# Kernel optimization log

Hardware: AMD Instinct MI355X
Metric: run time of the kernel (lower is better)

## Reference

```python
import jax, jax.numpy as jnp
import numpy as np

N_ATOM = 10000
D = 256
N_EDGE = 160000
BN_EPS = 1e-6


def _bn_eval(x, g, b, m, v):
    # BatchNorm1d in eval mode
    return (x - m) * jax.lax.rsqrt(v + BN_EPS) * g + b


def setup_inputs() -> dict:
    key = jax.random.key(0)
    ks = jax.random.split(key, 12)
    def glorot(k, shape):
        fan_in = shape[-1]
        return jax.random.normal(k, shape, dtype=jnp.float32) / np.sqrt(fan_in)
    inp = {
        'atom': jax.random.normal(ks[0], (N_ATOM, D), dtype=jnp.float32),
        'bond_index': jax.random.randint(ks[1], (2, N_EDGE), 0, N_ATOM, dtype=jnp.int32),
        # align: Linear(2D -> 1) + BN(1)
        'W_align': glorot(ks[2], (1, 2 * D)),
        'b_align': jnp.zeros((1,), jnp.float32),
        'bn_a_g': jnp.ones((1,), jnp.float32),
        'bn_a_b': jnp.zeros((1,), jnp.float32),
        'bn_a_m': jnp.zeros((1,), jnp.float32),
        'bn_a_v': jnp.ones((1,), jnp.float32),
        # attend: Linear(D -> D) + BN(D)
        'W_att': glorot(ks[3], (D, D)),
        'b_att': jnp.zeros((D,), jnp.float32),
        'bn_t_g': jnp.ones((D,), jnp.float32),
        'bn_t_b': jnp.zeros((D,), jnp.float32),
        'bn_t_m': jnp.zeros((D,), jnp.float32),
        'bn_t_v': jnp.ones((D,), jnp.float32),
        # GRUCell(D, D): weights stacked [r; z; n] as in torch
        'W_ih': glorot(ks[4], (3 * D, D)),
        'W_hh': glorot(ks[5], (3 * D, D)),
        'b_ih': jnp.zeros((3 * D,), jnp.float32),
        'b_hh': jnp.zeros((3 * D,), jnp.float32),
    }
    return inp


def reference(atom, bond_index, W_align, b_align, bn_a_g, bn_a_b, bn_a_m, bn_a_v,
              W_att, b_att, bn_t_g, bn_t_b, bn_t_m, bn_t_v,
              W_ih, W_hh, b_ih, b_hh):
    num_atom = atom.shape[0]
    src = bond_index[0]
    dst = bond_index[1]

    # gather + concat: [E, 2D]
    feat_align = jnp.concatenate([atom[src], atom[dst]], axis=-1)
    # align score: Linear(2D->1) + BN + leaky_relu -> [E, 1]
    s = feat_align @ W_align.T + b_align
    s = _bn_eval(s, bn_a_g, bn_a_b, bn_a_m, bn_a_v)
    s = jax.nn.leaky_relu(s, negative_slope=0.01)

    # segment softmax over edges grouped by src atom
    seg_max = jax.ops.segment_max(s, src, num_segments=num_atom)  # [N, 1]
    e = jnp.exp(s - seg_max[src])
    denom = jax.ops.segment_sum(e, src, num_segments=num_atom)    # [N, 1]
    attn = e / (denom[src] + 1e-8)                                # [E, 1]

    # attend: Linear(D->D) + BN on gathered dst features
    h = atom[dst] @ W_att.T + b_att
    h = _bn_eval(h, bn_t_g, bn_t_b, bn_t_m, bn_t_v)

    # weighted scatter-add aggregation -> [N, D], then ELU
    context = jax.ops.segment_sum(attn * h, src, num_segments=num_atom)
    context = jax.nn.elu(context)

    # GRUCell: input=context, hidden=atom
    gi = context @ W_ih.T + b_ih   # [N, 3D]
    gh = atom @ W_hh.T + b_hh      # [N, 3D]
    i_r, i_z, i_n = jnp.split(gi, 3, axis=-1)
    h_r, h_z, h_n = jnp.split(gh, 3, axis=-1)
    r = jax.nn.sigmoid(i_r + h_r)
    z = jax.nn.sigmoid(i_z + h_z)
    n = jnp.tanh(i_n + r * h_n)
    update = (1.0 - z) * n + z * atom
    return update
```

## Files before the change

kernel.cpp:

```cpp
#include <hip/hip_runtime.h>
#include <hip/hip_bf16.h>

#define D 256

typedef __attribute__((ext_vector_type(8))) short bf16x8;
typedef __attribute__((ext_vector_type(4))) short s16x4;
typedef __attribute__((ext_vector_type(4))) float f32x4;

#define MFMA __builtin_amdgcn_mfma_f32_16x16x32_bf16

__device__ __forceinline__ float s2f(short u) {
    union { unsigned int i; float f; } c;
    c.i = ((unsigned int)(unsigned short)u) << 16;
    return c.f;
}
__device__ __forceinline__ short f2s(float f) {
    union { float f; unsigned int u; } c; c.f = f;
    unsigned int u = c.u;
    u += 0x7fffu + ((u >> 16) & 1u);
    return (short)(u >> 16);
}

__global__ __launch_bounds__(256) void cvt_all_kernel(
    const float* __restrict__ atom, short* __restrict__ atom_bf, int nA,
    const float* __restrict__ Wa, short* __restrict__ Wa_bf, int nW,
    const float* __restrict__ Wi, short* __restrict__ Wi_bf,
    const float* __restrict__ Wh, short* __restrict__ Wh_bf, int nG)
{
    int i = blockIdx.x * 256 + threadIdx.x;
    const float* src; short* dst; int j = i;
    if (j < nA) { src = atom; dst = atom_bf; }
    else { j -= nA;
        if (j < nW) { src = Wa; dst = Wa_bf; }
        else { j -= nW;
            if (j < nG) { src = Wi; dst = Wi_bf; }
            else { j -= nG;
                if (j < nG) { src = Wh; dst = Wh_bf; }
                else return;
            }
        }
    }
    float4 v = ((const float4*)src)[j];
    s16x4 o; o[0] = f2s(v.x); o[1] = f2s(v.y); o[2] = f2s(v.z); o[3] = f2s(v.w);
    ((s16x4*)dst)[j] = o;
}

__global__ __launch_bounds__(256) void p0p1_kernel(
    const float* __restrict__ atom, const float* __restrict__ W_align,
    const float* __restrict__ b_align,
    const float* __restrict__ g, const float* __restrict__ bb,
    const float* __restrict__ mn, const float* __restrict__ vr,
    float* __restrict__ p0p, float* __restrict__ p1p, int N)
{
    int w = (blockIdx.x * blockDim.x + threadIdx.x) >> 6;
    int lane = threadIdx.x & 63;
    if (w >= N) return;
    float4 a  = *(const float4*)(atom + (size_t)w * D + lane * 4);
    float4 w0 = *(const float4*)(W_align + lane * 4);
    float4 w1 = *(const float4*)(W_align + D + lane * 4);
    float d0 = a.x * w0.x + a.y * w0.y + a.z * w0.z + a.w * w0.w;
    float d1 = a.x * w1.x + a.y * w1.y + a.z * w1.z + a.w * w1.w;
    #pragma unroll
    for (int o = 32; o > 0; o >>= 1) {
        d0 += __shfl_xor(d0, o, 64);
        d1 += __shfl_xor(d1, o, 64);
    }
    if (lane == 0) {
        float A = rsqrtf(vr[0] + 1e-6f) * g[0];
        p0p[w] = A * (d0 + b_align[0]) + bb[0] - A * mn[0];
        p1p[w] = A * d1;
    }
}

__global__ __launch_bounds__(256) void init_kernel(int* cnt, int* cursor, int N) {
    int i = blockIdx.x * 256 + threadIdx.x;
    if (i < N) { cnt[i] = 0; cursor[i] = 0; }
}

__global__ __launch_bounds__(256) void count_kernel(const int* __restrict__ src, int* cnt, int E) {
    int e = blockIdx.x * 256 + threadIdx.x;
    if (e < E) atomicAdd(&cnt[src[e]], 1);
}

__global__ __launch_bounds__(1024) void scan_kernel(const int* __restrict__ cnt, int* __restrict__ off, int N) {
    __shared__ int sums[1024];
    int t = threadIdx.x;
    int CH = (N + 1023) / 1024;
    int beg = t * CH;
    int end = beg + CH; if (end > N) end = N;
    int s = 0;
    for (int i = beg; i < end; i++) s += cnt[i];
    sums[t] = s;
    __syncthreads();
    for (int d = 1; d < 1024; d <<= 1) {
        int x = (t >= d) ? sums[t - d] : 0;
        __syncthreads();
        sums[t] += x;
        __syncthreads();
    }
    int run = (t > 0) ? sums[t - 1] : 0;
    for (int i = beg; i < end; i++) { off[i] = run; run += cnt[i]; }
    if (end == N) off[N] = run;
}

__global__ __launch_bounds__(256) void fill_kernel(const int* __restrict__ src, const int* __restrict__ dst,
                                                   const int* __restrict__ off, int* cursor, int* dlist, int E) {
    int e = blockIdx.x * 256 + threadIdx.x;
    if (e < E) {
        int s = src[e];
        int p = atomicAdd(&cursor[s], 1);
        dlist[off[s] + p] = dst[e];
    }
}

__global__ __launch_bounds__(256) void hA_kernel(
    const short* __restrict__ atom_bf, const short* __restrict__ W_bf,
    const float* __restrict__ bias,
    const float* __restrict__ g, const float* __restrict__ bb,
    const float* __restrict__ mn, const float* __restrict__ vr,
    short* __restrict__ hA, int N, int NB)
{
    __shared__ short Bs[64 * 264];
    int bi = blockIdx.x;
    int xcd = bi & 7, rest = bi >> 3;
    int cb = rest & 3, gh = rest >> 2;
    int gg = gh * 8 + xcd;
    if (gg >= NB) return;
    int c0 = cb * 64;
    int tid = threadIdx.x;
    for (int c = tid; c < 64 * 32; c += 256) {
        int row = c >> 5, o16 = c & 31;
        bf16x8 v = *(const bf16x8*)(W_bf + (size_t)(c0 + row) * D + o16 * 8);
        *(bf16x8*)(&Bs[row * 264 + o16 * 8]) = v;
    }
    __syncthreads();

    int wave = tid >> 6, lane = tid & 63;
    int quad = lane >> 4, l15 = lane & 15;
    int m0 = gg * 64 + wave * 16;
    int arow = m0 + l15; if (arow > N - 1) arow = N - 1;
    const short* ap = atom_bf + (size_t)arow * D + quad * 8;
    const short* b0p = &Bs[(l15) * 264 + quad * 8];
    const short* b1p = &Bs[(16 + l15) * 264 + quad * 8];
    const short* b2p = &Bs[(32 + l15) * 264 + quad * 8];
    const short* b3p = &Bs[(48 + l15) * 264 + quad * 8];
    f32x4 ac0 = {0,0,0,0}, ac1 = {0,0,0,0}, ac2 = {0,0,0,0}, ac3 = {0,0,0,0};
    #pragma unroll
    for (int k = 0; k < D; k += 32) {
        bf16x8 a  = *(const bf16x8*)(ap + k);
        bf16x8 b0 = *(const bf16x8*)(b0p + k);
        bf16x8 b1 = *(const bf16x8*)(b1p + k);
        bf16x8 b2 = *(const bf16x8*)(b2p + k);
        bf16x8 b3 = *(const bf16x8*)(b3p + k);
        ac0 = MFMA(a, b0, ac0, 0, 0, 0);
        ac1 = MFMA(a, b1, ac1, 0, 0, 0);
        ac2 = MFMA(a, b2, ac2, 0, 0, 0);
        ac3 = MFMA(a, b3, ac3, 0, 0, 0);
    }
    f32x4 accs[4] = {ac0, ac1, ac2, ac3};
    #pragma unroll
    for (int t = 0; t < 4; t++) {
        int col = c0 + t * 16 + l15;
        float sc = rsqrtf(vr[col] + 1e-6f) * g[col];
        float sh = bb[col] - mn[col] * sc;
        float bi_ = bias[col];
        #pragma unroll
        for (int r = 0; r < 4; r++) {
            int row = m0 + quad * 4 + r;
            if (row < N) hA[(size_t)row * D + col] = f2s((accs[t][r] + bi_) * sc + sh);
        }
    }
}

__global__ __launch_bounds__(256) void agg_kernel(
    const int* __restrict__ off, const int* __restrict__ dlist,
    const float* __restrict__ p0p, const float* __restrict__ p1p,
    const short* __restrict__ hA, short* __restrict__ ctx, int N)
{
    int w = (blockIdx.x * blockDim.x + threadIdx.x) >> 6;
    int lane = threadIdx.x & 63;
    if (w >= N) return;
    int beg = off[w], end = off[w + 1];
    float u = p0p[w];
    float m = -INFINITY;
    for (int j = beg + lane; j < end; j += 64) {
        float x = u + p1p[dlist[j]];
        x = x > 0.f ? x : 0.01f * x;
        m = fmaxf(m, x);
    }
    #pragma unroll
    for (int o = 32; o > 0; o >>= 1) m = fmaxf(m, __shfl_xor(m, o, 64));
    float sum = 0.f;
    for (int j = beg + lane; j < end; j += 64) {
        float x = u + p1p[dlist[j]];
        x = x > 0.f ? x : 0.01f * x;
        sum += __expf(x - m);
    }
    #pragma unroll
    for (int o = 32; o > 0; o >>= 1) sum += __shfl_xor(sum, o, 64);
    float inv = 1.f / (sum + 1e-8f);
    int half = lane >> 5, l32 = lane & 31;
    float acc[8] = {0.f,0.f,0.f,0.f,0.f,0.f,0.f,0.f};
    for (int j = beg + half; j < end; j += 2) {
        int d = dlist[j];
        float x = u + p1p[d];
        x = x > 0.f ? x : 0.01f * x;
        float coef = __expf(x - m) * inv;
        bf16x8 h = *(const bf16x8*)(hA + (size_t)d * D + l32 * 8);
        #pragma unroll
        for (int i = 0; i < 8; i++) acc[i] += coef * s2f(h[i]);
    }
    #pragma unroll
    for (int i = 0; i < 8; i++) acc[i] += __shfl_xor(acc[i], 32, 64);
    if (half == 0) {
        bf16x8 o;
        #pragma unroll
        for (int i = 0; i < 8; i++) {
            float v = acc[i];
            v = v > 0.f ? v : __expf(v) - 1.f;
            o[i] = f2s(v);
        }
        *(bf16x8*)(ctx + (size_t)w * D + l32 * 8) = o;
    }
}

__global__ __launch_bounds__(256) void gru_kernel(
    const short* __restrict__ ctx, const short* __restrict__ atom_bf,
    const float* __restrict__ atom_f,
    const short* __restrict__ W_ih, const short* __restrict__ W_hh,
    const float* __restrict__ b_ih, const float* __restrict__ b_hh,
    float* __restrict__ out, int N, int NB)
{
    __shared__ short Bs[6 * 16 * 264];
    int bi = blockIdx.x;
    int xcd = bi & 7, rest = bi >> 3;
    int cb = rest & 15, gh = rest >> 4;
    int gg = gh * 8 + xcd;
    if (gg >= NB) return;
    int c0 = cb * 16;
    int tid = threadIdx.x;
    for (int c = tid; c < 96 * 32; c += 256) {
        int row = c >> 5, o16 = c & 31;
        int gate = row >> 4, r = row & 15;
        const short* srcp = (gate < 3)
            ? W_ih + (size_t)(gate * 256 + c0 + r) * D + o16 * 8
            : W_hh + (size_t)((gate - 3) * 256 + c0 + r) * D + o16 * 8;
        bf16x8 v = *(const bf16x8*)srcp;
        *(bf16x8*)(&Bs[row * 264 + o16 * 8]) = v;
    }
    __syncthreads();

    int wave = tid >> 6, lane = tid & 63;
    int quad = lane >> 4, l15 = lane & 15;
    int m0 = gg * 64 + wave * 16;
    int arow = m0 + l15; if (arow > N - 1) arow = N - 1;
    const short* cp = ctx + (size_t)arow * D + quad * 8;
    const short* ap = atom_bf + (size_t)arow * D + quad * 8;
    const short* lb = &Bs[l15 * 264 + quad * 8];
    f32x4 ir = {0,0,0,0}, iz = {0,0,0,0}, in_ = {0,0,0,0};
    f32x4 hr = {0,0,0,0}, hz = {0,0,0,0}, hn = {0,0,0,0};
    #pragma unroll
    for (int k = 0; k < D; k += 32) {
        bf16x8 a1 = *(const bf16x8*)(cp + k);
        bf16x8 a2 = *(const bf16x8*)(ap + k);
        bf16x8 bir = *(const bf16x8*)(lb + 0 * 4224 + k);
        bf16x8 biz = *(const bf16x8*)(lb + 1 * 4224 + k);
        bf16x8 bin = *(const bf16x8*)(lb + 2 * 4224 + k);
        bf16x8 bhr = *(const bf16x8*)(lb + 3 * 4224 + k);
        bf16x8 bhz = *(const bf16x8*)(lb + 4 * 4224 + k);
        bf16x8 bhn = *(const bf16x8*)(lb + 5 * 4224 + k);
        ir  = MFMA(a1, bir, ir, 0, 0, 0);
        iz  = MFMA(a1, biz, iz, 0, 0, 0);
        in_ = MFMA(a1, bin, in_, 0, 0, 0);
        hr  = MFMA(a2, bhr, hr, 0, 0, 0);
        hz  = MFMA(a2, bhz, hz, 0, 0, 0);
        hn  = MFMA(a2, bhn, hn, 0, 0, 0);
    }
    int col = c0 + l15;
    float bir_s = b_ih[col], biz_s = b_ih[col + 256], bin_s = b_ih[col + 512];
    float bhr_s = b_hh[col], bhz_s = b_hh[col + 256], bhn_s = b_hh[col + 512];
    #pragma unroll
    for (int r = 0; r < 4; r++) {
        int row = m0 + quad * 4 + r;
        if (row < N) {
            float rr = 1.f / (1.f + __expf(-(ir[r] + bir_s + hr[r] + bhr_s)));
            float zz = 1.f / (1.f + __expf(-(iz[r] + biz_s + hz[r] + bhz_s)));
            float nn = tanhf(in_[r] + bin_s + rr * (hn[r] + bhn_s));
            float at = atom_f[(size_t)row * D + col];
            out[(size_t)row * D + col] = (1.f - zz) * nn + zz * at;
        }
    }
}

extern "C" void kernel_launch(void* const* d_in, const int* in_sizes, int n_in,
                              void* d_out, int out_size, void* d_ws, size_t ws_size,
                              hipStream_t stream) {
    const float* atom    = (const float*)d_in[0];
    const int*   bond    = (const int*)d_in[1];
    const float* W_align = (const float*)d_in[2];
    const float* b_align = (const float*)d_in[3];
    const float* bn_a_g  = (const float*)d_in[4];
    const float* bn_a_b  = (const float*)d_in[5];
    const float* bn_a_m  = (const float*)d_in[6];
    const float* bn_a_v  = (const float*)d_in[7];
    const float* W_att   = (const float*)d_in[8];
    const float* b_att   = (const float*)d_in[9];
    const float* bn_t_g  = (const float*)d_in[10];
    const float* bn_t_b  = (const float*)d_in[11];
    const float* bn_t_m  = (const float*)d_in[12];
    const float* bn_t_v  = (const float*)d_in[13];
    const float* W_ih    = (const float*)d_in[14];
    const float* W_hh    = (const float*)d_in[15];
    const float* b_ih    = (const float*)d_in[16];
    const float* b_hh    = (const float*)d_in[17];

    int N = in_sizes[0] / D;
    int E = in_sizes[1] / 2;
    const int* src = bond;
    const int* dst = bond + E;

    char* w = (char*)d_ws;
    size_t o = 0;
    auto alloc = [&](size_t bytes) {
        void* p = w + o;
        o = (o + bytes + 255) & ~(size_t)255;
        return p;
    };
    int*   cnt     = (int*)alloc((size_t)N * 4);
    int*   cursor  = (int*)alloc((size_t)N * 4);
    int*   offv    = (int*)alloc((size_t)(N + 1) * 4);
    int*   dlist   = (int*)alloc((size_t)E * 4);
    float* p0p     = (float*)alloc((size_t)N * 4);
    float* p1p     = (float*)alloc((size_t)N * 4);
    short* hA      = (short*)alloc((size_t)N * D * 2);
    short* ctx     = (short*)alloc((size_t)N * D * 2);
    short* atom_bf = (short*)alloc((size_t)N * D * 2);
    short* Watt_bf = (short*)alloc((size_t)D * D * 2);
    short* Wih_bf  = (short*)alloc((size_t)3 * D * D * 2);
    short* Whh_bf  = (short*)alloc((size_t)3 * D * D * 2);

    int nA = N * D / 4, nW = D * D / 4, nG = 3 * D * D / 4;
    int nTot = nA + nW + 2 * nG;
    cvt_all_kernel<<<(nTot + 255) / 256, 256, 0, stream>>>(
        atom, atom_bf, nA, W_att, Watt_bf, nW, W_ih, Wih_bf, W_hh, Whh_bf, nG);

    p0p1_kernel<<<((size_t)N * 64 + 255) / 256, 256, 0, stream>>>(
        atom, W_align, b_align, bn_a_g, bn_a_b, bn_a_m, bn_a_v, p0p, p1p, N);
    init_kernel<<<(N + 255) / 256, 256, 0, stream>>>(cnt, cursor, N);
    count_kernel<<<(E + 255) / 256, 256, 0, stream>>>(src, cnt, E);
    scan_kernel<<<1, 1024, 0, stream>>>(cnt, offv, N);
    fill_kernel<<<(E + 255) / 256, 256, 0, stream>>>(src, dst, offv, cursor, dlist, E);

    int NB = (N + 63) / 64;
    int GH = (NB + 7) / 8;
    hA_kernel<<<8 * 4 * GH, 256, 0, stream>>>(
        atom_bf, Watt_bf, b_att, bn_t_g, bn_t_b, bn_t_m, bn_t_v, hA, N, NB);
    agg_kernel<<<((size_t)N * 64 + 255) / 256, 256, 0, stream>>>(
        offv, dlist, p0p, p1p, hA, ctx, N);
    gru_kernel<<<8 * 16 * GH, 256, 0, stream>>>(
        ctx, atom_bf, atom, Wih_bf, Whh_bf, b_ih, b_hh, (float*)d_out, N, NB);
}
```

Before: 200.0 us.

## Fuse prep kernels and double per-wave row tiles in the GEMM kernels

```diff
diff --git a/kernel.cpp b/kernel.cpp
--- a/kernel.cpp
+++ b/kernel.cpp
@@ -21,59 +21,62 @@
     return (short)(u >> 16);
 }
 
-__global__ __launch_bounds__(256) void cvt_all_kernel(
-    const float* __restrict__ atom, short* __restrict__ atom_bf, int nA,
-    const float* __restrict__ Wa, short* __restrict__ Wa_bf, int nW,
+__global__ __launch_bounds__(256) void prep_kernel(
+    const float* __restrict__ atom, short* __restrict__ atom_bf,
+    const float* __restrict__ W_align, const float* __restrict__ b_align,
+    const float* __restrict__ g, const float* __restrict__ bb,
+    const float* __restrict__ mn, const float* __restrict__ vr,
+    float* __restrict__ p0p, float* __restrict__ p1p,
+    const float* __restrict__ Wa, short* __restrict__ Wa_bf,
     const float* __restrict__ Wi, short* __restrict__ Wi_bf,
-    const float* __restrict__ Wh, short* __restrict__ Wh_bf, int nG)
+    const float* __restrict__ Wh, short* __restrict__ Wh_bf,
+    int* __restrict__ cnt, int* __restrict__ cursor,
+    int N, int NROWB, int WCVTB)
 {
-    int i = blockIdx.x * 256 + threadIdx.x;
-    const float* src; short* dst; int j = i;
-    if (j < nA) { src = atom; dst = atom_bf; }
-    else { j -= nA;
-        if (j < nW) { src = Wa; dst = Wa_bf; }
-        else { j -= nW;
-            if (j < nG) { src = Wi; dst = Wi_bf; }
-            else { j -= nG;
-                if (j < nG) { src = Wh; dst = Wh_bf; }
+    int b = blockIdx.x, tid = threadIdx.x;
+    if (b < NROWB) {
+        int wave = tid >> 6, lane = tid & 63;
+        int row = b * 4 + wave;
+        if (row >= N) return;
+        float4 a = *(const float4*)(atom + (size_t)row * D + lane * 4);
+        s16x4 o; o[0] = f2s(a.x); o[1] = f2s(a.y); o[2] = f2s(a.z); o[3] = f2s(a.w);
+        ((s16x4*)(atom_bf + (size_t)row * D))[lane] = o;
+        float4 w0 = *(const float4*)(W_align + lane * 4);
+        float4 w1 = *(const float4*)(W_align + D + lane * 4);
+        float d0 = a.x * w0.x + a.y * w0.y + a.z * w0.z + a.w * w0.w;
+        float d1 = a.x * w1.x + a.y * w1.y + a.z * w1.z + a.w * w1.w;
+        #pragma unroll
+        for (int s = 32; s > 0; s >>= 1) {
+            d0 += __shfl_xor(d0, s, 64);
+            d1 += __shfl_xor(d1, s, 64);
+        }
+        if (lane == 0) {
+            float A = rsqrtf(vr[0] + 1e-6f) * g[0];
+            p0p[row] = A * (d0 + b_align[0]) + bb[0] - A * mn[0];
+            p1p[row] = A * d1;
+        }
+        return;
+    }
+    b -= NROWB;
+    if (b < WCVTB) {
+        int nW4 = D * D / 4, nG4 = 3 * D * D / 4;
+        int j = b * 256 + tid;
+        const float* src; short* dst;
+        if (j < nW4) { src = Wa; dst = Wa_bf; }
+        else { j -= nW4;
+            if (j < nG4) { src = Wi; dst = Wi_bf; }
+            else { j -= nG4;
+                if (j < nG4) { src = Wh; dst = Wh_bf; }
                 else return;
             }
         }
-    }
-    float4 v = ((const float4*)src)[j];
-    s16x4 o; o[0] = f2s(v.x); o[1] = f2s(v.y); o[2] = f2s(v.z); o[3] = f2s(v.w);
-    ((s16x4*)dst)[j] = o;
-}
-
-__global__ __launch_bounds__(256) void p0p1_kernel(
-    const float* __restrict__ atom, const float* __restrict__ W_align,
-    const float* __restrict__ b_align,
-    const float* __restrict__ g, const float* __restrict__ bb,
-    const float* __restrict__ mn, const float* __restrict__ vr,
-    float* __restrict__ p0p, float* __restrict__ p1p, int N)
-{
-    int w = (blockIdx.x * blockDim.x + threadIdx.x) >> 6;
-    int lane = threadIdx.x & 63;
-    if (w >= N) return;
-    float4 a  = *(const float4*)(atom + (size_t)w * D + lane * 4);
-    float4 w0 = *(const float4*)(W_align + lane * 4);
-    float4 w1 = *(const float4*)(W_align + D + lane * 4);
-    float d0 = a.x * w0.x + a.y * w0.y + a.z * w0.z + a.w * w0.w;
-    float d1 = a.x * w1.x + a.y * w1.y + a.z * w1.z + a.w * w1.w;
-    #pragma unroll
-    for (int o = 32; o > 0; o >>= 1) {
-        d0 += __shfl_xor(d0, o, 64);
-        d1 += __shfl_xor(d1, o, 64);
-    }
-    if (lane == 0) {
-        float A = rsqrtf(vr[0] + 1e-6f) * g[0];
-        p0p[w] = A * (d0 + b_align[0]) + bb[0] - A * mn[0];
-        p1p[w] = A * d1;
-    }
-}
-
-__global__ __launch_bounds__(256) void init_kernel(int* cnt, int* cursor, int N) {
-    int i = blockIdx.x * 256 + threadIdx.x;
+        float4 v = ((const float4*)src)[j];
+        s16x4 o; o[0] = f2s(v.x); o[1] = f2s(v.y); o[2] = f2s(v.z); o[3] = f2s(v.w);
+        ((s16x4*)dst)[j] = o;
+        return;
+    }
+    b -= WCVTB;
+    int i = b * 256 + tid;
     if (i < N) { cnt[i] = 0; cursor[i] = 0; }
 }
 
@@ -137,37 +140,50 @@
 
     int wave = tid >> 6, lane = tid & 63;
     int quad = lane >> 4, l15 = lane & 15;
-    int m0 = gg * 64 + wave * 16;
-    int arow = m0 + l15; if (arow > N - 1) arow = N - 1;
-    const short* ap = atom_bf + (size_t)arow * D + quad * 8;
+    int m0 = gg * 128 + wave * 16;
+    int ar0 = m0 + l15;       if (ar0 > N - 1) ar0 = N - 1;
+    int ar1 = m0 + 64 + l15;  if (ar1 > N - 1) ar1 = N - 1;
+    const short* ap0 = atom_bf + (size_t)ar0 * D + quad * 8;
+    const short* ap1 = atom_bf + (size_t)ar1 * D + quad * 8;
     const short* b0p = &Bs[(l15) * 264 + quad * 8];
     const short* b1p = &Bs[(16 + l15) * 264 + quad * 8];
     const short* b2p = &Bs[(32 + l15) * 264 + quad * 8];
     const short* b3p = &Bs[(48 + l15) * 264 + quad * 8];
-    f32x4 ac0 = {0,0,0,0}, ac1 = {0,0,0,0}, ac2 = {0,0,0,0}, ac3 = {0,0,0,0};
+    f32x4 acc[2][4];
+    #pragma unroll
+    for (int t = 0; t < 2; t++)
+        #pragma unroll
+        for (int j = 0; j < 4; j++) acc[t][j] = (f32x4){0,0,0,0};
     #pragma unroll
     for (int k = 0; k < D; k += 32) {
-        bf16x8 a  = *(const bf16x8*)(ap + k);
+        bf16x8 a0 = *(const bf16x8*)(ap0 + k);
+        bf16x8 a1 = *(const bf16x8*)(ap1 + k);
         bf16x8 b0 = *(const bf16x8*)(b0p + k);
         bf16x8 b1 = *(const bf16x8*)(b1p + k);
         bf16x8 b2 = *(const bf16x8*)(b2p + k);
         bf16x8 b3 = *(const bf16x8*)(b3p + k);
-        ac0 = MFMA(a, b0, ac0, 0, 0, 0);
-        ac1 = MFMA(a, b1, ac1, 0, 0, 0);
-        ac2 = MFMA(a, b2, ac2, 0, 0, 0);
-        ac3 = MFMA(a, b3, ac3, 0, 0, 0);
-    }
-    f32x4 accs[4] = {ac0, ac1, ac2, ac3};
-    #pragma unroll
-    for (int t = 0; t < 4; t++) {
-        int col = c0 + t * 16 + l15;
+        acc[0][0] = MFMA(a0, b0, acc[0][0], 0, 0, 0);
+        acc[0][1] = MFMA(a0, b1, acc[0][1], 0, 0, 0);
+        acc[0][2] = MFMA(a0, b2, acc[0][2], 0, 0, 0);
+        acc[0][3] = MFMA(a0, b3, acc[0][3], 0, 0, 0);
+        acc[1][0] = MFMA(a1, b0, acc[1][0], 0, 0, 0);
+        acc[1][1] = MFMA(a1, b1, acc[1][1], 0, 0, 0);
+        acc[1][2] = MFMA(a1, b2, acc[1][2], 0, 0, 0);
+        acc[1][3] = MFMA(a1, b3, acc[1][3], 0, 0, 0);
+    }
+    #pragma unroll
+    for (int j = 0; j < 4; j++) {
+        int col = c0 + j * 16 + l15;
         float sc = rsqrtf(vr[col] + 1e-6f) * g[col];
         float sh = bb[col] - mn[col] * sc;
         float bi_ = bias[col];
         #pragma unroll
-        for (int r = 0; r < 4; r++) {
-            int row = m0 + quad * 4 + r;
-            if (row < N) hA[(size_t)row * D + col] = f2s((accs[t][r] + bi_) * sc + sh);
+        for (int t = 0; t < 2; t++) {
+            #pragma unroll
+            for (int r = 0; r < 4; r++) {
+                int row = m0 + t * 64 + quad * 4 + r;
+                if (row < N) hA[(size_t)row * D + col] = f2s((acc[t][j][r] + bi_) * sc + sh);
+            }
         }
     }
 }
@@ -252,42 +268,59 @@
 
     int wave = tid >> 6, lane = tid & 63;
     int quad = lane >> 4, l15 = lane & 15;
-    int m0 = gg * 64 + wave * 16;
-    int arow = m0 + l15; if (arow > N - 1) arow = N - 1;
-    const short* cp = ctx + (size_t)arow * D + quad * 8;
-    const short* ap = atom_bf + (size_t)arow * D + quad * 8;
+    int m0 = gg * 128 + wave * 16;
+    int ar0 = m0 + l15;       if (ar0 > N - 1) ar0 = N - 1;
+    int ar1 = m0 + 64 + l15;  if (ar1 > N - 1) ar1 = N - 1;
+    const short* cp0 = ctx + (size_t)ar0 * D + quad * 8;
+    const short* ap0 = atom_bf + (size_t)ar0 * D + quad * 8;
+    const short* cp1 = ctx + (size_t)ar1 * D + quad * 8;
+    const short* ap1 = atom_bf + (size_t)ar1 * D + quad * 8;
     const short* lb = &Bs[l15 * 264 + quad * 8];
-    f32x4 ir = {0,0,0,0}, iz = {0,0,0,0}, in_ = {0,0,0,0};
-    f32x4 hr = {0,0,0,0}, hz = {0,0,0,0}, hn = {0,0,0,0};
+    f32x4 gi[2][3], gh_[2][3];
+    #pragma unroll
+    for (int t = 0; t < 2; t++)
+        #pragma unroll
+        for (int j = 0; j < 3; j++) { gi[t][j] = (f32x4){0,0,0,0}; gh_[t][j] = (f32x4){0,0,0,0}; }
     #pragma unroll
     for (int k = 0; k < D; k += 32) {
-        bf16x8 a1 = *(const bf16x8*)(cp + k);
-        bf16x8 a2 = *(const bf16x8*)(ap + k);
+        bf16x8 c0v = *(const bf16x8*)(cp0 + k);
+        bf16x8 a0v = *(const bf16x8*)(ap0 + k);
+        bf16x8 c1v = *(const bf16x8*)(cp1 + k);
+        bf16x8 a1v = *(const bf16x8*)(ap1 + k);
         bf16x8 bir = *(const bf16x8*)(lb + 0 * 4224 + k);
         bf16x8 biz = *(const bf16x8*)(lb + 1 * 4224 + k);
         bf16x8 bin = *(const bf16x8*)(lb + 2 * 4224 + k);
         bf16x8 bhr = *(const bf16x8*)(lb + 3 * 4224 + k);
         bf16x8 bhz = *(const bf16x8*)(lb + 4 * 4224 + k);
         bf16x8 bhn = *(const bf16x8*)(lb + 5 * 4224 + k);
-        ir  = MFMA(a1, bir, ir, 0, 0, 0);
-        iz  = MFMA(a1, biz, iz, 0, 0, 0);
-        in_ = MFMA(a1, bin, in_, 0, 0, 0);
-        hr  = MFMA(a2, bhr, hr, 0, 0, 0);
-        hz  = MFMA(a2, bhz, hz, 0, 0, 0);
-        hn  = MFMA(a2, bhn, hn, 0, 0, 0);
+        gi[0][0] = MFMA(c0v, bir, gi[0][0], 0, 0, 0);
+        gi[0][1] = MFMA(c0v, biz, gi[0][1], 0, 0, 0);
+        gi[0][2] = MFMA(c0v, bin, gi[0][2], 0, 0, 0);
+        gh_[0][0] = MFMA(a0v, bhr, gh_[0][0], 0, 0, 0);
+        gh_[0][1] = MFMA(a0v, bhz, gh_[0][1], 0, 0, 0);
+        gh_[0][2] = MFMA(a0v, bhn, gh_[0][2], 0, 0, 0);
+        gi[1][0] = MFMA(c1v, bir, gi[1][0], 0, 0, 0);
+        gi[1][1] = MFMA(c1v, biz, gi[1][1], 0, 0, 0);
+        gi[1][2] = MFMA(c1v, bin, gi[1][2], 0, 0, 0);
+        gh_[1][0] = MFMA(a1v, bhr, gh_[1][0], 0, 0, 0);
+        gh_[1][1] = MFMA(a1v, bhz, gh_[1][1], 0, 0, 0);
+        gh_[1][2] = MFMA(a1v, bhn, gh_[1][2], 0, 0, 0);
     }
     int col = c0 + l15;
     float bir_s = b_ih[col], biz_s = b_ih[col + 256], bin_s = b_ih[col + 512];
     float bhr_s = b_hh[col], bhz_s = b_hh[col + 256], bhn_s = b_hh[col + 512];
     #pragma unroll
-    for (int r = 0; r < 4; r++) {
-        int row = m0 + quad * 4 + r;
-        if (row < N) {
-            float rr = 1.f / (1.f + __expf(-(ir[r] + bir_s + hr[r] + bhr_s)));
-            float zz = 1.f / (1.f + __expf(-(iz[r] + biz_s + hz[r] + bhz_s)));
-            float nn = tanhf(in_[r] + bin_s + rr * (hn[r] + bhn_s));
-            float at = atom_f[(size_t)row * D + col];
-            out[(size_t)row * D + col] = (1.f - zz) * nn + zz * at;
+    for (int t = 0; t < 2; t++) {
+        #pragma unroll
+        for (int r = 0; r < 4; r++) {
+            int row = m0 + t * 64 + quad * 4 + r;
+            if (row < N) {
+                float rr = 1.f / (1.f + __expf(-(gi[t][0][r] + bir_s + gh_[t][0][r] + bhr_s)));
+                float zz = 1.f / (1.f + __expf(-(gi[t][1][r] + biz_s + gh_[t][1][r] + bhz_s)));
+                float nn = tanhf(gi[t][2][r] + bin_s + rr * (gh_[t][2][r] + bhn_s));
+                float at = atom_f[(size_t)row * D + col];
+                out[(size_t)row * D + col] = (1.f - zz) * nn + zz * at;
+            }
         }
     }
 }
@@ -339,19 +372,18 @@
     short* Wih_bf  = (short*)alloc((size_t)3 * D * D * 2);
     short* Whh_bf  = (short*)alloc((size_t)3 * D * D * 2);
 
-    int nA = N * D / 4, nW = D * D / 4, nG = 3 * D * D / 4;
-    int nTot = nA + nW + 2 * nG;
-    cvt_all_kernel<<<(nTot + 255) / 256, 256, 0, stream>>>(
-        atom, atom_bf, nA, W_att, Watt_bf, nW, W_ih, Wih_bf, W_hh, Whh_bf, nG);
-
-    p0p1_kernel<<<((size_t)N * 64 + 255) / 256, 256, 0, stream>>>(
-        atom, W_align, b_align, bn_a_g, bn_a_b, bn_a_m, bn_a_v, p0p, p1p, N);
-    init_kernel<<<(N + 255) / 256, 256, 0, stream>>>(cnt, cursor, N);
+    int NROWB = (N + 3) / 4;
+    int nWtot4 = (D * D + 2 * 3 * D * D) / 4;
+    int WCVTB = (nWtot4 + 255) / 256;
+    int INITB = (N + 255) / 256;
+    prep_kernel<<<NROWB + WCVTB + INITB, 256, 0, stream>>>(
+        atom, atom_bf, W_align, b_align, bn_a_g, bn_a_b, bn_a_m, bn_a_v, p0p, p1p,
+        W_att, Watt_bf, W_ih, Wih_bf, W_hh, Whh_bf, cnt, cursor, N, NROWB, WCVTB);
     count_kernel<<<(E + 255) / 256, 256, 0, stream>>>(src, cnt, E);
     scan_kernel<<<1, 1024, 0, stream>>>(cnt, offv, N);
     fill_kernel<<<(E + 255) / 256, 256, 0, stream>>>(src, dst, offv, cursor, dlist, E);
 
-    int NB = (N + 63) / 64;
+    int NB = (N + 127) / 128;
     int GH = (NB + 7) / 8;
     hA_kernel<<<8 * 4 * GH, 256, 0, stream>>>(
         atom_bf, Watt_bf, b_att, bn_t_g, bn_t_b, bn_t_m, bn_t_v, hA, N, NB);
```

Measured after the change: 201.0 us. About the same (+0.5%).
